# Performance work log

Hardware: AMD Instinct MI355X
Metric: run time of the kernel (lower is better)

## Reference

```python
import jax, jax.numpy as jnp
import numpy as np

B, S, D_IN, D_E = 8, 2048, 1024, 1024


def setup_inputs() -> dict:
    key = jax.random.key(0)
    ks = jax.random.split(key, 9)
    s_in = 1.0 / np.sqrt(D_IN)
    s_e = 1.0 / np.sqrt(D_E)
    return {
        "x": jax.random.normal(ks[0], (B, S, D_IN), dtype=jnp.float32),
        "Wq": jax.random.uniform(ks[1], (D_IN, D_E), jnp.float32, -s_in, s_in),
        "bq": jax.random.uniform(ks[2], (D_E,), jnp.float32, -s_in, s_in),
        "Wk": jax.random.uniform(ks[3], (D_IN, D_E), jnp.float32, -s_in, s_in),
        "bk": jax.random.uniform(ks[4], (D_E,), jnp.float32, -s_in, s_in),
        "Wv": jax.random.uniform(ks[5], (D_IN, D_E), jnp.float32, -s_in, s_in),
        "bv": jax.random.uniform(ks[6], (D_E,), jnp.float32, -s_in, s_in),
        "Wo": jax.random.uniform(ks[7], (D_E, D_E), jnp.float32, -s_e, s_e),
        "bo": jax.random.uniform(ks[8], (D_E,), jnp.float32, -s_e, s_e),
    }


def reference(x, Wq, bq, Wk, bk, Wv, bv, Wo, bo):
    # QKV projections: [B,S,D_in] @ [D_in,D_e] -> [B,S,D_e]
    Q = jnp.einsum("bsi,ie->bse", x, Wq) + bq
    K = jnp.einsum("bsi,ie->bse", x, Wk) + bk
    V = jnp.einsum("bsi,ie->bse", x, Wv) + bv
    scale = 1.0 / jnp.sqrt(jnp.asarray(Q.shape[-1], Q.dtype))
    # full score matrix [B,S,S] (faithful to the unfused original)
    logits = jnp.einsum("bqe,bke->bqk", Q, K) * scale
    attn = jax.nn.softmax(logits, axis=-1)
    values = jnp.einsum("bqk,bke->bqe", attn, V)
    o = jnp.einsum("bqe,ef->bqf", values, Wo) + bo
    return o
```

## Files before the change

### kernel.cpp

```cpp
#include <hip/hip_runtime.h>

#define DIN 1024
#define DE  1024
#define SEQ 2048
#define NB  8

typedef __bf16 bf16x8 __attribute__((ext_vector_type(8)));
typedef float  f32x4  __attribute__((ext_vector_type(4)));
typedef unsigned short u16;
typedef u16 u16x8 __attribute__((ext_vector_type(8)));
typedef u16 u16x4 __attribute__((ext_vector_type(4)));

__device__ __forceinline__ u16 f2bf(float f) {
  unsigned u = __builtin_bit_cast(unsigned, f);
  return (u16)((u + 0x7FFFu + ((u >> 16) & 1u)) >> 16);
}
__device__ __forceinline__ float bf2f(u16 h) {
  return __builtin_bit_cast(float, (unsigned)h << 16);
}

typedef __attribute__((address_space(1))) const unsigned char g_u8;
typedef __attribute__((address_space(3))) unsigned char l_u8;
__device__ __forceinline__ void gload16(const void* g, void* l) {
  __builtin_amdgcn_global_load_lds((g_u8*)g, (l_u8*)l, 16, 0, 0);
}

__device__ __forceinline__ int swz_addr(int r, int g) {
  return (r >> 1) * 128 + (((((r & 1) << 2) | g) ^ ((r >> 1) & 7)) << 4);
}
__device__ __forceinline__ void swz_decode(int S, int& r, int& g) {
  const int pr = S >> 3, phys = S & 7, inner = phys ^ (pr & 7);
  r = pr * 2 + (inner >> 2);
  g = inner & 3;
}

__global__ __launch_bounds__(256) void cvt_f32_bf16(const float* __restrict__ in,
                                                    u16* __restrict__ out, int n4) {
  int i = blockIdx.x * 256 + threadIdx.x;
  if (i >= n4) return;
  float4 v = ((const float4*)in)[i];
  u16x4 o;
  o[0] = f2bf(v.x); o[1] = f2bf(v.y); o[2] = f2bf(v.z); o[3] = f2bf(v.w);
  ((u16x4*)out)[i] = o;
}

__global__ __launch_bounds__(256) void transpose_w(const float* __restrict__ W,
                                                   u16* __restrict__ Wt) {
  __shared__ float t[32][33];
  const int tx = threadIdx.x, ty = threadIdx.y;
  const int bx = blockIdx.x * 32, by = blockIdx.y * 32;
#pragma unroll
  for (int i = 0; i < 4; ++i)
    t[ty + i * 8][tx] = W[(size_t)(by + ty + i * 8) * 1024 + bx + tx];
  __syncthreads();
#pragma unroll
  for (int i = 0; i < 4; ++i)
    Wt[(size_t)(bx + ty + i * 8) * 1024 + by + tx] = f2bf(t[tx][ty + i * 8]);
}

__global__ __launch_bounds__(256) void softmax_rows_bf16(u16* __restrict__ P) {
  const size_t row = blockIdx.x;
  u16* pr = P + row * 2048 + (size_t)threadIdx.x * 8;
  u16x8 v = *(const u16x8*)pr;
  float x[8];
#pragma unroll
  for (int j = 0; j < 8; ++j) x[j] = bf2f(v[j]);
  float m = x[0];
#pragma unroll
  for (int j = 1; j < 8; ++j) m = fmaxf(m, x[j]);
#pragma unroll
  for (int off = 32; off; off >>= 1) m = fmaxf(m, __shfl_xor(m, off));
  __shared__ float rm[4], rs[4];
  const int lane = threadIdx.x & 63, wid = threadIdx.x >> 6;
  if (lane == 0) rm[wid] = m;
  __syncthreads();
  m = fmaxf(fmaxf(rm[0], rm[1]), fmaxf(rm[2], rm[3]));
  float s = 0.f;
#pragma unroll
  for (int j = 0; j < 8; ++j) { x[j] = __expf(x[j] - m); s += x[j]; }
#pragma unroll
  for (int off = 32; off; off >>= 1) s += __shfl_xor(s, off);
  if (lane == 0) rs[wid] = s;
  __syncthreads();
  s = (rs[0] + rs[1]) + (rs[2] + rs[3]);
  const float inv = 1.f / s;
  u16x8 o;
#pragma unroll
  for (int j = 0; j < 8; ++j) o[j] = f2bf(x[j] * inv);
  *(u16x8*)pr = o;
}

template <int BMT, int OMODE, bool HAS_BIAS>
__global__ __launch_bounds__(512, 1) void gemm8p(
    const u16* __restrict__ A, const u16* __restrict__ Bt, void* __restrict__ Cv,
    const float* __restrict__ bias, int M, int N, int K,
    size_t sA, size_t sB, size_t sC, float scale) {
  constexpr int ABYTES = BMT * 64;
  constexpr int BUFB = ABYTES + 16384;
  constexpr int MR = BMT >> 5;
  constexpr int LA = BMT >> 7;
  __shared__ __align__(16) char lds8[4 * BUFB];
  const int tid = threadIdx.x, lane = tid & 63, wid = tid >> 6;
  const int wm = wid >> 2, wn = wid & 3;

  const int gx = gridDim.x, gy = gridDim.y;
  int lin = blockIdx.x + gx * (blockIdx.y + gy * blockIdx.z);
  const int nwg = gx * gy * (int)gridDim.z;
  const int q = nwg >> 3, r8 = nwg & 7;
  const int xcd = lin & 7, idx = lin >> 3;
  lin = (xcd < r8 ? xcd * (q + 1) : r8 * (q + 1) + (xcd - r8) * q) + idx;
  const int bz = lin / (gx * gy);
  const int rem = lin - bz * (gx * gy);
  const int by = rem / gx, bx = rem - (rem / gx) * gx;

  const char* Ag = (const char*)(A + (size_t)bz * sA + (size_t)by * BMT * K);
  const char* Bg = (const char*)(Bt + (size_t)bz * sB + (size_t)bx * 256 * K);
  const size_t Kb = (size_t)K * 2;

  const char* srcA[2];
  const char* srcB[2];
  char* dstA[2];
  char* dstB[2];
#pragma unroll
  for (int j = 0; j < LA; ++j) {
    int S = (j * 8 + wid) * 64 + lane, r, g;
    swz_decode(S, r, g);
    srcA[j] = Ag + (size_t)r * Kb + g * 16;
    dstA[j] = lds8 + (j * 8 + wid) * 1024;
  }
#pragma unroll
  for (int j = 0; j < 2; ++j) {
    int S = (j * 8 + wid) * 64 + lane, r, g;
    swz_decode(S, r, g);
    srcB[j] = Bg + (size_t)r * Kb + g * 16;
    dstB[j] = lds8 + ABYTES + (j * 8 + wid) * 1024;
  }

  const int lane15 = lane & 15, gk = lane >> 4;
  int aoff[MR], boff[4];
#pragma unroll
  for (int m = 0; m < MR; ++m)
    aoff[m] = swz_addr(wm * (BMT / 2) + m * 16 + lane15, gk);
#pragma unroll
  for (int n = 0; n < 4; ++n)
    boff[n] = ABYTES + swz_addr(wn * 64 + n * 16 + lane15, gk);

  f32x4 acc[MR][4] = {};
  const int NT = K >> 5;

#pragma unroll
  for (int pt = 0; pt < 3; ++pt) {
    const int bb = pt * BUFB;
#pragma unroll
    for (int j = 0; j < LA; ++j) { gload16(srcA[j], dstA[j] + bb); srcA[j] += 64; }
#pragma unroll
    for (int j = 0; j < 2; ++j) { gload16(srcB[j], dstB[j] + bb); srcB[j] += 64; }
  }
  if constexpr (BMT == 256) asm volatile("s_waitcnt vmcnt(8)" ::: "memory");
  else                      asm volatile("s_waitcnt vmcnt(6)" ::: "memory");
  __builtin_amdgcn_s_barrier();
  __builtin_amdgcn_sched_barrier(0);

  for (int t = 0; t < NT; ++t) {
    const char* base = lds8 + (t & 3) * BUFB;
    const int dbb = ((t + 3) & 3) * BUFB;
    const bool st = (t + 3) < NT;
    bf16x8 af[4], bfr[4];
#pragma unroll
    for (int n = 0; n < 4; ++n) bfr[n] = *(const bf16x8*)(base + boff[n]);
#pragma unroll
    for (int m = 0; m < 4; ++m) af[m] = *(const bf16x8*)(base + aoff[m]);
    if constexpr (BMT == 256) {
      if (st) {
        gload16(srcA[0], dstA[0] + dbb); srcA[0] += 64;
        gload16(srcA[1], dstA[1] + dbb); srcA[1] += 64;
      }
      __builtin_amdgcn_s_setprio(1);
#pragma unroll
      for (int m = 0; m < 4; ++m)
#pragma unroll
        for (int n = 0; n < 4; ++n)
          acc[m][n] = __builtin_amdgcn_mfma_f32_16x16x32_bf16(af[m], bfr[n], acc[m][n], 0, 0, 0);
      __builtin_amdgcn_s_setprio(0);
      __builtin_amdgcn_s_barrier();
#pragma unroll
      for (int m = 0; m < 4; ++m) af[m] = *(const bf16x8*)(base + aoff[4 + m]);
      if (st) {
        gload16(srcB[0], dstB[0] + dbb); srcB[0] += 64;
        gload16(srcB[1], dstB[1] + dbb); srcB[1] += 64;
      }
      __builtin_amdgcn_s_setprio(1);
#pragma unroll
      for (int m = 0; m < 4; ++m)
#pragma unroll
        for (int n = 0; n < 4; ++n)
          acc[4 + m][n] = __builtin_amdgcn_mfma_f32_16x16x32_bf16(af[m], bfr[n], acc[4 + m][n], 0, 0, 0);
      __builtin_amdgcn_s_setprio(0);
      if (t < NT - 3)       asm volatile("s_waitcnt vmcnt(8)" ::: "memory");
      else if (t == NT - 3) asm volatile("s_waitcnt vmcnt(4)" ::: "memory");
      else if (t == NT - 2) asm volatile("s_waitcnt vmcnt(0)" ::: "memory");
    } else {
      if (st) {
        gload16(srcA[0], dstA[0] + dbb); srcA[0] += 64;
        gload16(srcB[0], dstB[0] + dbb); srcB[0] += 64;
        gload16(srcB[1], dstB[1] + dbb); srcB[1] += 64;
      }
      __builtin_amdgcn_s_setprio(1);
#pragma unroll
      for (int m = 0; m < 4; ++m)
#pragma unroll
        for (int n = 0; n < 4; ++n)
          acc[m][n] = __builtin_amdgcn_mfma_f32_16x16x32_bf16(af[m], bfr[n], acc[m][n], 0, 0, 0);
      __builtin_amdgcn_s_setprio(0);
      if (t < NT - 3)       asm volatile("s_waitcnt vmcnt(6)" ::: "memory");
      else if (t == NT - 3) asm volatile("s_waitcnt vmcnt(3)" ::: "memory");
      else if (t == NT - 2) asm volatile("s_waitcnt vmcnt(0)" ::: "memory");
    }
    __builtin_amdgcn_s_barrier();
    __builtin_amdgcn_sched_barrier(0);
  }

  const int rbase = by * BMT + wm * (BMT / 2) + ((lane >> 4) << 2);
  const int cbase = bx * 256 + wn * 64 + lane15;
#pragma unroll
  for (int m = 0; m < MR; ++m)
#pragma unroll
    for (int n = 0; n < 4; ++n) {
      const int col = cbase + n * 16;
      const float bval = HAS_BIAS ? bias[col] : 0.f;
#pragma unroll
      for (int r = 0; r < 4; ++r) {
        const int rowg = rbase + m * 16 + r;
        const float v = acc[m][n][r] * scale + bval;
        if (OMODE == 0)
          ((float*)Cv)[(size_t)bz * sC + (size_t)rowg * N + col] = v;
        else if (OMODE == 1)
          ((u16*)Cv)[(size_t)bz * sC + (size_t)rowg * N + col] = f2bf(v);
        else
          ((u16*)Cv)[(size_t)(rowg >> 11) * ((size_t)DE * SEQ) +
                     (size_t)col * SEQ + (rowg & 2047)] = f2bf(v);
      }
    }
}

extern "C" void kernel_launch(void* const* d_in, const int* in_sizes, int n_in,
                              void* d_out, int out_size, void* d_ws, size_t ws_size,
                              hipStream_t stream) {
  const float* x  = (const float*)d_in[0];
  const float* Wq = (const float*)d_in[1];
  const float* bq = (const float*)d_in[2];
  const float* Wk = (const float*)d_in[3];
  const float* bk = (const float*)d_in[4];
  const float* Wv = (const float*)d_in[5];
  const float* bv = (const float*)d_in[6];
  const float* Wo = (const float*)d_in[7];
  const float* bo = (const float*)d_in[8];

  const size_t NEED = 150994944;
  if (ws_size < NEED) return;
  char* ws = (char*)d_ws;
  u16* x_bf = (u16*)(ws);
  u16* q_bf = (u16*)(ws + 33554432);
  u16* k_bf = (u16*)(ws + 67108864);
  u16* vt   = (u16*)(ws + 100663296);
  u16* wt   = (u16*)(ws + 134217728);
  u16* lgP  = x_bf;
  u16* wt_q = wt;
  u16* wt_k = wt + 1048576;
  u16* wt_v = wt + 2097152;
  u16* wt_o = wt + 3145728;

  dim3 tb(32, 8);
  const size_t sQ = (size_t)SEQ * DE;
  const size_t sL = (size_t)1024 * SEQ;

  cvt_f32_bf16<<<16384, 256, 0, stream>>>(x, x_bf, (NB * SEQ * DIN) / 4);
  transpose_w<<<dim3(32, 32), tb, 0, stream>>>(Wq, wt_q);
  transpose_w<<<dim3(32, 32), tb, 0, stream>>>(Wk, wt_k);
  transpose_w<<<dim3(32, 32), tb, 0, stream>>>(Wv, wt_v);
  transpose_w<<<dim3(32, 32), tb, 0, stream>>>(Wo, wt_o);
  gemm8p<256, 1, true><<<dim3(4, 64, 1), 512, 0, stream>>>(x_bf, wt_q, q_bf, bq,
      16384, 1024, 1024, 0, 0, 0, 1.f);
  gemm8p<256, 1, true><<<dim3(4, 64, 1), 512, 0, stream>>>(x_bf, wt_k, k_bf, bk,
      16384, 1024, 1024, 0, 0, 0, 1.f);
  gemm8p<256, 2, true><<<dim3(4, 64, 1), 512, 0, stream>>>(x_bf, wt_v, vt, bv,
      16384, 1024, 1024, 0, 0, 0, 1.f);
  for (int c = 0; c < 2; ++c) {
    const u16* qc = q_bf + (size_t)c * 1048576;
    gemm8p<128, 1, false><<<dim3(8, 8, 8), 512, 0, stream>>>(qc, k_bf, lgP, nullptr,
        1024, 2048, 1024, sQ, sQ, sL, 0.03125f);
    softmax_rows_bf16<<<8192, 256, 0, stream>>>(lgP);
    gemm8p<128, 1, false><<<dim3(4, 8, 8), 512, 0, stream>>>(lgP, vt,
        q_bf + (size_t)c * 1048576, nullptr, 1024, 1024, 2048, sL, sQ, sQ, 1.f);
  }
  gemm8p<256, 0, true><<<dim3(4, 64, 1), 512, 0, stream>>>(q_bf, wt_o, d_out, bo,
      16384, 1024, 1024, 0, 0, 0, 1.f);

  (void)in_sizes; (void)n_in; (void)out_size; (void)ws_size;
}
```

Baseline: 369.3 us.

## Rewrite GEMM mainloop with K=64 double-buffered tiles and phased half-tile staging

Replaces the 4-stage, K=32-per-step GEMM pipeline with a 2-buffer, K=64-per-step scheme. Global-to-LDS loads for A and the two B halves are interleaved between four MFMA phases, with barriers and lgkmcnt waits between them. The LDS layout moves to a simpler XOR swizzle on 128-byte rows. The aim is to halve loop and barrier overhead per unit of K and overlap loads with compute more finely. In exchange it adds more barriers per iteration and leaves less prefetch depth, which could expose global latency.

```diff
diff --git a/kernel.cpp b/kernel.cpp
--- a/kernel.cpp
+++ b/kernel.cpp
@@ -23,15 +23,6 @@
 typedef __attribute__((address_space(3))) unsigned char l_u8;
 __device__ __forceinline__ void gload16(const void* g, void* l) {
   __builtin_amdgcn_global_load_lds((g_u8*)g, (l_u8*)l, 16, 0, 0);
-}
-
-__device__ __forceinline__ int swz_addr(int r, int g) {
-  return (r >> 1) * 128 + (((((r & 1) << 2) | g) ^ ((r >> 1) & 7)) << 4);
-}
-__device__ __forceinline__ void swz_decode(int S, int& r, int& g) {
-  const int pr = S >> 3, phys = S & 7, inner = phys ^ (pr & 7);
-  r = pr * 2 + (inner >> 2);
-  g = inner & 3;
 }
 
 __global__ __launch_bounds__(256) void cvt_f32_bf16(const float* __restrict__ in,
@@ -91,17 +82,19 @@
 }
 
 template <int BMT, int OMODE, bool HAS_BIAS>
-__global__ __launch_bounds__(512, 1) void gemm8p(
+__global__ __launch_bounds__(512, 1) void gemmph(
     const u16* __restrict__ A, const u16* __restrict__ Bt, void* __restrict__ Cv,
     const float* __restrict__ bias, int M, int N, int K,
     size_t sA, size_t sB, size_t sC, float scale) {
-  constexpr int ABYTES = BMT * 64;
-  constexpr int BUFB = ABYTES + 16384;
-  constexpr int MR = BMT >> 5;
-  constexpr int LA = BMT >> 7;
-  __shared__ __align__(16) char lds8[4 * BUFB];
+  constexpr int ABYTES = BMT * 128;
+  constexpr int AHALF  = ABYTES / 2;
+  constexpr int BUFB   = ABYTES + 32768;
+  constexpr int LA     = AHALF / 8192;
+  constexpr int MR     = BMT / 32;
+  __shared__ __align__(16) char lds8[2 * BUFB];
   const int tid = threadIdx.x, lane = tid & 63, wid = tid >> 6;
   const int wm = wid >> 2, wn = wid & 3;
+  const int lane15 = lane & 15, gk = lane >> 4;
 
   const int gx = gridDim.x, gy = gridDim.y;
   int lin = blockIdx.x + gx * (blockIdx.y + gy * blockIdx.z);
@@ -117,110 +110,182 @@
   const char* Bg = (const char*)(Bt + (size_t)bz * sB + (size_t)bx * 256 * K);
   const size_t Kb = (size_t)K * 2;
 
-  const char* srcA[2];
-  const char* srcB[2];
-  char* dstA[2];
-  char* dstB[2];
-#pragma unroll
-  for (int j = 0; j < LA; ++j) {
-    int S = (j * 8 + wid) * 64 + lane, r, g;
-    swz_decode(S, r, g);
-    srcA[j] = Ag + (size_t)r * Kb + g * 16;
-    dstA[j] = lds8 + (j * 8 + wid) * 1024;
+  const int spr = tid >> 3;
+  const int sg = (tid & 7) ^ (spr & 7);
+  const char* srcA[2][2];
+  const char* srcB[2][2];
+#pragma unroll
+  for (int h = 0; h < 2; ++h) {
+#pragma unroll
+    for (int j = 0; j < LA; ++j)
+      srcA[h][j] = Ag + (size_t)(h * (BMT / 2) + j * 64 + spr) * Kb + sg * 16;
+#pragma unroll
+    for (int j = 0; j < 2; ++j)
+      srcB[h][j] = Bg + (size_t)(h * 128 + j * 64 + spr) * Kb + sg * 16;
   }
-#pragma unroll
-  for (int j = 0; j < 2; ++j) {
-    int S = (j * 8 + wid) * 64 + lane, r, g;
-    swz_decode(S, r, g);
-    srcB[j] = Bg + (size_t)r * Kb + g * 16;
-    dstB[j] = lds8 + ABYTES + (j * 8 + wid) * 1024;
-  }
-
-  const int lane15 = lane & 15, gk = lane >> 4;
-  int aoff[MR], boff[4];
-#pragma unroll
-  for (int m = 0; m < MR; ++m)
-    aoff[m] = swz_addr(wm * (BMT / 2) + m * 16 + lane15, gk);
-#pragma unroll
-  for (int n = 0; n < 4; ++n)
-    boff[n] = ABYTES + swz_addr(wn * 64 + n * 16 + lane15, gk);
+
+  auto stageA2 = [&](int dbuf) {
+#pragma unroll
+    for (int h = 0; h < 2; ++h) {
+      char* d = lds8 + dbuf * BUFB + h * AHALF + tid * 16;
+#pragma unroll
+      for (int j = 0; j < LA; ++j) { gload16(srcA[h][j], d + j * 8192); srcA[h][j] += 128; }
+    }
+  };
+  auto stageB1 = [&](int h, int dbuf) {
+    char* d = lds8 + dbuf * BUFB + ABYTES + h * 16384 + tid * 16;
+    gload16(srcB[h][0], d);        srcB[h][0] += 128;
+    gload16(srcB[h][1], d + 8192); srcB[h][1] += 128;
+  };
+
+  const int arow = lane15 * 128 + ((gk ^ (lane15 & 7)) << 4);
 
   f32x4 acc[MR][4] = {};
-  const int NT = K >> 5;
-
-#pragma unroll
-  for (int pt = 0; pt < 3; ++pt) {
-    const int bb = pt * BUFB;
-#pragma unroll
-    for (int j = 0; j < LA; ++j) { gload16(srcA[j], dstA[j] + bb); srcA[j] += 64; }
-#pragma unroll
-    for (int j = 0; j < 2; ++j) { gload16(srcB[j], dstB[j] + bb); srcB[j] += 64; }
-  }
-  if constexpr (BMT == 256) asm volatile("s_waitcnt vmcnt(8)" ::: "memory");
-  else                      asm volatile("s_waitcnt vmcnt(6)" ::: "memory");
+  const int NT = K >> 6;
+
+  stageA2(0); stageB1(0, 0); stageB1(1, 0);
+  stageB1(0, 1); stageA2(1);
+  if constexpr (BMT == 256) asm volatile("s_waitcnt vmcnt(6)" ::: "memory");
+  else                      asm volatile("s_waitcnt vmcnt(4)" ::: "memory");
   __builtin_amdgcn_s_barrier();
   __builtin_amdgcn_sched_barrier(0);
 
-  for (int t = 0; t < NT; ++t) {
-    const char* base = lds8 + (t & 3) * BUFB;
-    const int dbb = ((t + 3) & 3) * BUFB;
-    const bool st = (t + 3) < NT;
-    bf16x8 af[4], bfr[4];
-#pragma unroll
-    for (int n = 0; n < 4; ++n) bfr[n] = *(const bf16x8*)(base + boff[n]);
-#pragma unroll
-    for (int m = 0; m < 4; ++m) af[m] = *(const bf16x8*)(base + aoff[m]);
+  for (int kt = 0; kt < NT; ++kt) {
+    const char* Ab = lds8 + (kt & 1) * BUFB + wm * AHALF;
+    const char* Bb = lds8 + (kt & 1) * BUFB + ABYTES + (wn >> 1) * 16384 + (wn & 1) * 8192;
+    const int nbuf = (kt + 1) & 1;
+    const int cbuf = kt & 1;
+    bf16x8 af[4][2], bfr[4][2];
+
     if constexpr (BMT == 256) {
-      if (st) {
-        gload16(srcA[0], dstA[0] + dbb); srcA[0] += 64;
-        gload16(srcA[1], dstA[1] + dbb); srcA[1] += 64;
-      }
-      __builtin_amdgcn_s_setprio(1);
-#pragma unroll
-      for (int m = 0; m < 4; ++m)
-#pragma unroll
-        for (int n = 0; n < 4; ++n)
-          acc[m][n] = __builtin_amdgcn_mfma_f32_16x16x32_bf16(af[m], bfr[n], acc[m][n], 0, 0, 0);
-      __builtin_amdgcn_s_setprio(0);
-      __builtin_amdgcn_s_barrier();
-#pragma unroll
-      for (int m = 0; m < 4; ++m) af[m] = *(const bf16x8*)(base + aoff[4 + m]);
-      if (st) {
-        gload16(srcB[0], dstB[0] + dbb); srcB[0] += 64;
-        gload16(srcB[1], dstB[1] + dbb); srcB[1] += 64;
-      }
-      __builtin_amdgcn_s_setprio(1);
-#pragma unroll
-      for (int m = 0; m < 4; ++m)
-#pragma unroll
-        for (int n = 0; n < 4; ++n)
-          acc[4 + m][n] = __builtin_amdgcn_mfma_f32_16x16x32_bf16(af[m], bfr[n], acc[4 + m][n], 0, 0, 0);
-      __builtin_amdgcn_s_setprio(0);
-      if (t < NT - 3)       asm volatile("s_waitcnt vmcnt(8)" ::: "memory");
-      else if (t == NT - 3) asm volatile("s_waitcnt vmcnt(4)" ::: "memory");
-      else if (t == NT - 2) asm volatile("s_waitcnt vmcnt(0)" ::: "memory");
+#pragma unroll
+      for (int m = 0; m < 4; ++m) {
+        af[m][0] = *(const bf16x8*)(Ab + m * 2048 + arow);
+        af[m][1] = *(const bf16x8*)(Ab + m * 2048 + (arow ^ 64));
+      }
+#pragma unroll
+      for (int n = 0; n < 2; ++n) {
+        bfr[n][0] = *(const bf16x8*)(Bb + n * 2048 + arow);
+        bfr[n][1] = *(const bf16x8*)(Bb + n * 2048 + (arow ^ 64));
+      }
+      if (kt + 1 < NT) stageB1(1, nbuf);
+      __builtin_amdgcn_s_barrier();
+      asm volatile("s_waitcnt lgkmcnt(0)" ::: "memory");
+      __builtin_amdgcn_sched_barrier(0);
+      __builtin_amdgcn_s_setprio(1);
+#pragma unroll
+      for (int m = 0; m < 4; ++m)
+#pragma unroll
+        for (int n = 0; n < 2; ++n) {
+          acc[m][n] = __builtin_amdgcn_mfma_f32_16x16x32_bf16(af[m][0], bfr[n][0], acc[m][n], 0, 0, 0);
+          acc[m][n] = __builtin_amdgcn_mfma_f32_16x16x32_bf16(af[m][1], bfr[n][1], acc[m][n], 0, 0, 0);
+        }
+      __builtin_amdgcn_s_setprio(0);
+      __builtin_amdgcn_s_barrier();
+      __builtin_amdgcn_sched_barrier(0);
+#pragma unroll
+      for (int n = 2; n < 4; ++n) {
+        bfr[n][0] = *(const bf16x8*)(Bb + n * 2048 + arow);
+        bfr[n][1] = *(const bf16x8*)(Bb + n * 2048 + (arow ^ 64));
+      }
+      __builtin_amdgcn_s_barrier();
+      asm volatile("s_waitcnt lgkmcnt(0)" ::: "memory");
+      __builtin_amdgcn_sched_barrier(0);
+      __builtin_amdgcn_s_setprio(1);
+#pragma unroll
+      for (int m = 0; m < 4; ++m)
+#pragma unroll
+        for (int n = 2; n < 4; ++n) {
+          acc[m][n] = __builtin_amdgcn_mfma_f32_16x16x32_bf16(af[m][0], bfr[n][0], acc[m][n], 0, 0, 0);
+          acc[m][n] = __builtin_amdgcn_mfma_f32_16x16x32_bf16(af[m][1], bfr[n][1], acc[m][n], 0, 0, 0);
+        }
+      __builtin_amdgcn_s_setprio(0);
+      __builtin_amdgcn_s_barrier();
+      __builtin_amdgcn_sched_barrier(0);
+#pragma unroll
+      for (int m = 0; m < 4; ++m) {
+        af[m][0] = *(const bf16x8*)(Ab + (4 + m) * 2048 + arow);
+        af[m][1] = *(const bf16x8*)(Ab + (4 + m) * 2048 + (arow ^ 64));
+      }
+      if (kt + 2 < NT) stageB1(0, cbuf);
+      __builtin_amdgcn_s_barrier();
+      asm volatile("s_waitcnt lgkmcnt(0)" ::: "memory");
+      __builtin_amdgcn_sched_barrier(0);
+      __builtin_amdgcn_s_setprio(1);
+#pragma unroll
+      for (int m = 0; m < 4; ++m)
+#pragma unroll
+        for (int n = 0; n < 2; ++n) {
+          acc[4 + m][n] = __builtin_amdgcn_mfma_f32_16x16x32_bf16(af[m][0], bfr[n][0], acc[4 + m][n], 0, 0, 0);
+          acc[4 + m][n] = __builtin_amdgcn_mfma_f32_16x16x32_bf16(af[m][1], bfr[n][1], acc[4 + m][n], 0, 0, 0);
+        }
+      __builtin_amdgcn_s_setprio(0);
+      __builtin_amdgcn_s_barrier();
+      __builtin_amdgcn_sched_barrier(0);
+      if (kt + 2 < NT) stageA2(cbuf);
+      __builtin_amdgcn_s_barrier();
+      asm volatile("s_waitcnt lgkmcnt(0)" ::: "memory");
+      __builtin_amdgcn_sched_barrier(0);
+      __builtin_amdgcn_s_setprio(1);
+#pragma unroll
+      for (int m = 0; m < 4; ++m)
+#pragma unroll
+        for (int n = 2; n < 4; ++n) {
+          acc[4 + m][n] = __builtin_amdgcn_mfma_f32_16x16x32_bf16(af[m][0], bfr[n][0], acc[4 + m][n], 0, 0, 0);
+          acc[4 + m][n] = __builtin_amdgcn_mfma_f32_16x16x32_bf16(af[m][1], bfr[n][1], acc[4 + m][n], 0, 0, 0);
+        }
+      __builtin_amdgcn_s_setprio(0);
+      if (kt < NT - 2)      asm volatile("s_waitcnt vmcnt(6)" ::: "memory");
+      else if (kt == NT - 2) asm volatile("s_waitcnt vmcnt(0)" ::: "memory");
+      __builtin_amdgcn_s_barrier();
+      __builtin_amdgcn_sched_barrier(0);
     } else {
-      if (st) {
-        gload16(srcA[0], dstA[0] + dbb); srcA[0] += 64;
-        gload16(srcB[0], dstB[0] + dbb); srcB[0] += 64;
-        gload16(srcB[1], dstB[1] + dbb); srcB[1] += 64;
-      }
-      __builtin_amdgcn_s_setprio(1);
-#pragma unroll
-      for (int m = 0; m < 4; ++m)
-#pragma unroll
-        for (int n = 0; n < 4; ++n)
-          acc[m][n] = __builtin_amdgcn_mfma_f32_16x16x32_bf16(af[m], bfr[n], acc[m][n], 0, 0, 0);
-      __builtin_amdgcn_s_setprio(0);
-      if (t < NT - 3)       asm volatile("s_waitcnt vmcnt(6)" ::: "memory");
-      else if (t == NT - 3) asm volatile("s_waitcnt vmcnt(3)" ::: "memory");
-      else if (t == NT - 2) asm volatile("s_waitcnt vmcnt(0)" ::: "memory");
+#pragma unroll
+      for (int m = 0; m < 4; ++m) {
+        af[m][0] = *(const bf16x8*)(Ab + m * 2048 + arow);
+        af[m][1] = *(const bf16x8*)(Ab + m * 2048 + (arow ^ 64));
+      }
+#pragma unroll
+      for (int n = 0; n < 4; ++n) {
+        bfr[n][0] = *(const bf16x8*)(Bb + n * 2048 + arow);
+        bfr[n][1] = *(const bf16x8*)(Bb + n * 2048 + (arow ^ 64));
+      }
+      if (kt + 1 < NT) stageB1(1, nbuf);
+      __builtin_amdgcn_s_barrier();
+      asm volatile("s_waitcnt lgkmcnt(0)" ::: "memory");
+      __builtin_amdgcn_sched_barrier(0);
+      __builtin_amdgcn_s_setprio(1);
+#pragma unroll
+      for (int m = 0; m < 4; ++m)
+#pragma unroll
+        for (int n = 0; n < 2; ++n) {
+          acc[m][n] = __builtin_amdgcn_mfma_f32_16x16x32_bf16(af[m][0], bfr[n][0], acc[m][n], 0, 0, 0);
+          acc[m][n] = __builtin_amdgcn_mfma_f32_16x16x32_bf16(af[m][1], bfr[n][1], acc[m][n], 0, 0, 0);
+        }
+      __builtin_amdgcn_s_setprio(0);
+      __builtin_amdgcn_s_barrier();
+      __builtin_amdgcn_sched_barrier(0);
+      if (kt + 2 < NT) { stageA2(cbuf); stageB1(0, cbuf); }
+      __builtin_amdgcn_s_barrier();
+      asm volatile("s_waitcnt lgkmcnt(0)" ::: "memory");
+      __builtin_amdgcn_sched_barrier(0);
+      __builtin_amdgcn_s_setprio(1);
+#pragma unroll
+      for (int m = 0; m < 4; ++m)
+#pragma unroll
+        for (int n = 2; n < 4; ++n) {
+          acc[m][n] = __builtin_amdgcn_mfma_f32_16x16x32_bf16(af[m][0], bfr[n][0], acc[m][n], 0, 0, 0);
+          acc[m][n] = __builtin_amdgcn_mfma_f32_16x16x32_bf16(af[m][1], bfr[n][1], acc[m][n], 0, 0, 0);
+        }
+      __builtin_amdgcn_s_setprio(0);
+      if (kt < NT - 2)      asm volatile("s_waitcnt vmcnt(4)" ::: "memory");
+      else if (kt == NT - 2) asm volatile("s_waitcnt vmcnt(0)" ::: "memory");
+      __builtin_amdgcn_s_barrier();
+      __builtin_amdgcn_sched_barrier(0);
     }
-    __builtin_amdgcn_s_barrier();
-    __builtin_amdgcn_sched_barrier(0);
   }
 
-  const int rbase = by * BMT + wm * (BMT / 2) + ((lane >> 4) << 2);
+  const int rbase = by * BMT + wm * (BMT / 2) + (gk << 2);
   const int cbase = bx * 256 + wn * 64 + lane15;
 #pragma unroll
   for (int m = 0; m < MR; ++m)
@@ -279,21 +344,21 @@
   transpose_w<<<dim3(32, 32), tb, 0, stream>>>(Wk, wt_k);
   transpose_w<<<dim3(32, 32), tb, 0, stream>>>(Wv, wt_v);
   transpose_w<<<dim3(32, 32), tb, 0, stream>>>(Wo, wt_o);
-  gemm8p<256, 1, true><<<dim3(4, 64, 1), 512, 0, stream>>>(x_bf, wt_q, q_bf, bq,
+  gemmph<256, 1, true><<<dim3(4, 64, 1), 512, 0, stream>>>(x_bf, wt_q, q_bf, bq,
       16384, 1024, 1024, 0, 0, 0, 1.f);
-  gemm8p<256, 1, true><<<dim3(4, 64, 1), 512, 0, stream>>>(x_bf, wt_k, k_bf, bk,
+  gemmph<256, 1, true><<<dim3(4, 64, 1), 512, 0, stream>>>(x_bf, wt_k, k_bf, bk,
       16384, 1024, 1024, 0, 0, 0, 1.f);
-  gemm8p<256, 2, true><<<dim3(4, 64, 1), 512, 0, stream>>>(x_bf, wt_v, vt, bv,
+  gemmph<256, 2, true><<<dim3(4, 64, 1), 512, 0, stream>>>(x_bf, wt_v, vt, bv,
       16384, 1024, 1024, 0, 0, 0, 1.f);
   for (int c = 0; c < 2; ++c) {
     const u16* qc = q_bf + (size_t)c * 1048576;
-    gemm8p<128, 1, false><<<dim3(8, 8, 8), 512, 0, stream>>>(qc, k_bf, lgP, nullptr,
+    gemmph<128, 1, false><<<dim3(8, 8, 8), 512, 0, stream>>>(qc, k_bf, lgP, nullptr,
         1024, 2048, 1024, sQ, sQ, sL, 0.03125f);
     softmax_rows_bf16<<<8192, 256, 0, stream>>>(lgP);
-    gemm8p<128, 1, false><<<dim3(4, 8, 8), 512, 0, stream>>>(lgP, vt,
+    gemmph<128, 1, false><<<dim3(4, 8, 8), 512, 0, stream>>>(lgP, vt,
         q_bf + (size_t)c * 1048576, nullptr, 1024, 1024, 2048, sL, sQ, sQ, 1.f);
   }
-  gemm8p<256, 0, true><<<dim3(4, 64, 1), 512, 0, stream>>>(q_bf, wt_o, d_out, bo,
+  gemmph<256, 0, true><<<dim3(4, 64, 1), 512, 0, stream>>>(q_bf, wt_o, d_out, bo,
       16384, 1024, 1024, 0, 0, 0, 1.f);
 
   (void)in_sizes; (void)n_in; (void)out_size; (void)ws_size;
```

New measurement: 376.6 us. About the same (+2.0%).
